# Kernel tuning notes

Hardware: AMD Instinct MI355X
Metric: run time of the kernel (lower is better)

## Reference

```python
import jax, jax.numpy as jnp
import numpy as np

NEG_SLOPE = 0.01  # torch F.leaky_relu default

def _leaky(x):
    return jnp.where(x >= 0, x, NEG_SLOPE * x)

def _gcn(x, W, b, src, dst, w, n):
    # GCNConv(add_self_loops=False, normalize=False):
    # h = x @ W; out[dst] += w * h[src]; out += b
    h = x @ W
    agg = jax.ops.segment_sum(w[:, None] * h[src], dst, num_segments=n)
    return agg + b

def setup_inputs() -> dict:
    key = jax.random.key(0)
    ks = jax.random.split(key, 10)
    N, E, IN, HID, OUT, B = 100000, 300000, 256, 256, 256, 128
    features = jax.random.normal(ks[0], (N, IN), dtype=jnp.float32)
    values = jax.random.uniform(ks[1], (E,), dtype=jnp.float32)
    s = 1.0 / np.sqrt(IN)
    W1 = jax.random.normal(ks[2], (IN, HID), dtype=jnp.float32) * s
    b1 = jnp.zeros((HID,), dtype=jnp.float32)
    W2 = jax.random.normal(ks[3], (HID + IN, OUT), dtype=jnp.float32) * (1.0 / np.sqrt(HID + IN))
    b2 = jnp.zeros((OUT,), dtype=jnp.float32)
    Wl = jax.random.normal(ks[4], (HID + OUT, IN), dtype=jnp.float32) * (1.0 / np.sqrt(HID + OUT))
    bl = jnp.zeros((IN,), dtype=jnp.float32)
    adjs = jax.random.randint(ks[5], (2, E), 0, N, dtype=jnp.int64)
    batch = jnp.sort(jax.random.randint(ks[6], (N,), 0, B, dtype=jnp.int64))
    root_idx = jax.random.randint(ks[7], (B,), 0, N, dtype=jnp.int64)
    return {"features": features, "values": values, "W1": W1, "b1": b1,
            "W2": W2, "b2": b2, "Wl": Wl, "bl": bl,
            "adjs": adjs, "batch": batch, "root_idx": root_idx}

def reference(features, values, W1, b1, W2, b2, Wl, bl, adjs, batch, root_idx):
    N = features.shape[0]
    src, dst = adjs[0], adjs[1]
    f1 = features  # [N, in]
    h = _gcn(f1, W1, b1, src, dst, values, N)  # conv1 -> [N, hid]
    f2 = h
    # root_extend: per-batch broadcast of root features == gather f1[root_idx[batch]]
    root1 = f1[root_idx[batch]]  # [N, in]
    x = _leaky(jnp.concatenate([h, root1], axis=1))
    # dropout is identity at inference
    x = _gcn(x, W2, b2, src, dst, values, N)  # conv2 -> [N, out]
    x = _leaky(x)
    root2 = f2[root_idx[batch]]  # [N, hid]
    x = jnp.concatenate([x, root2], axis=1)
    return _leaky(x @ Wl + bl)  # [N, in]
```

## Files before the change

### kernel.cpp

```cpp
#include <hip/hip_runtime.h>

typedef short short8 __attribute__((ext_vector_type(8)));
typedef float floatx4 __attribute__((ext_vector_type(4)));

#define LEAKY(v) ((v) >= 0.0f ? (v) : 0.01f * (v))

constexpr int D = 256;

__device__ __forceinline__ short f2bf(float x) {
  unsigned u = __float_as_uint(x);
  u += 0x7fffu + ((u >> 16) & 1u);
  return (short)(u >> 16);
}
__device__ __forceinline__ float bf2f(short s) {
  return __uint_as_float(((unsigned)(unsigned short)s) << 16);
}

#define AS1 __attribute__((address_space(1)))
#define AS3 __attribute__((address_space(3)))

__device__ __forceinline__ void gload_lds16(const void* g, void* lds) {
  __builtin_amdgcn_global_load_lds((const AS1 void*)g, (AS3 void*)lds, 16, 0, 0);
}

__global__ void transpose_w(const float* __restrict__ W1,
                            const float* __restrict__ W2,
                            const float* __restrict__ Wl,
                            short* __restrict__ Wt) {
  __shared__ float t[32][33];
  const float* src = (blockIdx.z == 0) ? W1 : (blockIdx.z == 1) ? W2 : Wl;
  short* dst = Wt + (size_t)blockIdx.z * D * D;
  int tx = threadIdx.x, ty = threadIdx.y;
  t[ty][tx] = src[(size_t)(blockIdx.y * 32 + ty) * D + blockIdx.x * 32 + tx];
  __syncthreads();
  dst[(size_t)(blockIdx.x * 32 + ty) * D + blockIdx.y * 32 + tx] =
      f2bf(t[tx][ty]);
}

template <bool A_F32, bool ADD_ROW, bool FINAL>
__global__ __launch_bounds__(512, 2) void gemm_pipe(
    const void* __restrict__ Avoid, const short* __restrict__ Wt,
    const float* __restrict__ R, const int* __restrict__ batch,
    const float* __restrict__ bias, void* __restrict__ Cvoid, int M,
    int nTiles) {
  constexpr int TB = A_F32 ? 32768 : 16384;
  __shared__ __align__(16) char As[2][TB];
  const int tid = threadIdx.x;
  const int l = tid & 63, w = tid >> 6, lm = l & 15, q = l >> 4;
  const int ncol0 = w * 32;

  short8 bf[2][8];
#pragma unroll
  for (int j = 0; j < 2; j++)
#pragma unroll
    for (int kk = 0; kk < 8; kk++)
      bf[j][kk] = *(const short8*)(Wt + (size_t)(ncol0 + j * 16 + lm) * D +
                                   kk * 32 + q * 8);
#pragma unroll
  for (int j = 0; j < 2; j++)
#pragma unroll
    for (int kk = 0; kk < 8; kk++)
      asm volatile("" : "+v"(bf[j][kk]));

  float4 b4[2];
  if (FINAL) {
#pragma unroll
    for (int j = 0; j < 2; j++)
      b4[j] = *(const float4*)(bias + ncol0 + j * 16 + q * 4);
  }

  const int stride = gridDim.x;
  int t = blockIdx.x;
  int p = 0;

  auto stage = [&](int tile, int buf) {
    if (A_F32) {
#pragma unroll
      for (int r = 0; r < 4; r++) {
        const int c = r * 8 + w;
        const int s = c >> 1, h = c & 1;
        const int kk = s >> 1, i = s & 1;
        int grow = tile * 32 + i * 16 + lm;
        grow = grow < M ? grow : M - 1;
        const char* src = (const char*)Avoid + (size_t)grow * 1024 +
                          kk * 128 + q * 32 + h * 16;
        gload_lds16(src, &As[buf][s * 2048 + h * 1024]);
      }
    } else {
#pragma unroll
      for (int r = 0; r < 2; r++) {
        const int s = r * 8 + w;
        const int kk = s >> 1, i = s & 1;
        int grow = tile * 32 + i * 16 + lm;
        grow = grow < M ? grow : M - 1;
        const char* src =
            (const char*)Avoid + (size_t)grow * 512 + kk * 64 + q * 16;
        gload_lds16(src, &As[buf][s * 1024]);
      }
    }
  };

  if (t < nTiles) stage(t, 0);

  for (; t < nTiles; t += stride) {
    __syncthreads();
    const int nxt = t + stride;
    if (nxt < nTiles) stage(nxt, p ^ 1);

    floatx4 acc[2][2];
#pragma unroll
    for (int i = 0; i < 2; i++)
#pragma unroll
      for (int j = 0; j < 2; j++) acc[i][j] = (floatx4){0.f, 0.f, 0.f, 0.f};

    const char* base = &As[p][0] + (size_t)l * 16;
#pragma unroll
    for (int kk = 0; kk < 8; kk++) {
      short8 a[2];
#pragma unroll
      for (int i = 0; i < 2; i++) {
        if (A_F32) {
          const int s = kk * 2 + i;
          float4 lo = *(const float4*)(base + s * 2048);
          float4 hi = *(const float4*)(base + s * 2048 + 1024);
          short8 sv;
          sv[0] = f2bf(lo.x); sv[1] = f2bf(lo.y); sv[2] = f2bf(lo.z); sv[3] = f2bf(lo.w);
          sv[4] = f2bf(hi.x); sv[5] = f2bf(hi.y); sv[6] = f2bf(hi.z); sv[7] = f2bf(hi.w);
          a[i] = sv;
        } else {
          a[i] = *(const short8*)(base + (kk * 2 + i) * 1024);
        }
      }
#pragma unroll
      for (int i = 0; i < 2; i++)
#pragma unroll
        for (int j = 0; j < 2; j++)
          acc[i][j] = __builtin_amdgcn_mfma_f32_16x16x32_bf16(
              bf[j][kk], a[i], acc[i][j], 0, 0, 0);
    }

    const int rowBase = t * 32;
#pragma unroll
    for (int i = 0; i < 2; i++) {
      const int row = rowBase + i * 16 + lm;
      if (row < M) {
        int rb = 0;
        if (ADD_ROW) rb = batch[row];
#pragma unroll
        for (int j = 0; j < 2; j++) {
          const int col0 = ncol0 + j * 16 + q * 4;
          float c0 = acc[i][j][0], c1 = acc[i][j][1], c2 = acc[i][j][2],
                c3 = acc[i][j][3];
          if (ADD_ROW) {
            float4 rv = *(const float4*)(R + (size_t)rb * D + col0);
            c0 += rv.x; c1 += rv.y; c2 += rv.z; c3 += rv.w;
          }
          if (!FINAL) {
            uint2 o;
            o.x = (unsigned)(unsigned short)f2bf(c0) |
                  ((unsigned)(unsigned short)f2bf(c1) << 16);
            o.y = (unsigned)(unsigned short)f2bf(c2) |
                  ((unsigned)(unsigned short)f2bf(c3) << 16);
            *(uint2*)((short*)Cvoid + (size_t)row * D + col0) = o;
          } else {
            c0 += b4[j].x; c1 += b4[j].y; c2 += b4[j].z; c3 += b4[j].w;
            c0 = LEAKY(c0); c1 = LEAKY(c1); c2 = LEAKY(c2); c3 = LEAKY(c3);
            float4 o = {c0, c1, c2, c3};
            *(float4*)((float*)Cvoid + (size_t)row * D + col0) = o;
          }
        }
      }
    }
    p ^= 1;
  }
}

__global__ void count_dst(const int* __restrict__ dst, int* __restrict__ offs,
                          int E) {
  int e = blockIdx.x * 256 + threadIdx.x;
  if (e < E) atomicAdd(&offs[dst[e]], 1);
}

__global__ void scan_blocks(int* __restrict__ offs, int* __restrict__ bsums,
                            int n) {
  __shared__ int tmp[256];
  int i = blockIdx.x * 256 + threadIdx.x;
  int v = (i < n) ? offs[i] : 0;
  tmp[threadIdx.x] = v;
  __syncthreads();
  for (int off = 1; off < 256; off <<= 1) {
    int t = (threadIdx.x >= off) ? tmp[threadIdx.x - off] : 0;
    __syncthreads();
    tmp[threadIdx.x] += t;
    __syncthreads();
  }
  if (i < n) offs[i] = tmp[threadIdx.x] - v;
  if (threadIdx.x == 255) bsums[blockIdx.x] = tmp[255];
}

__global__ void scan_sums(int* __restrict__ bs, int nb) {
  __shared__ int tmp[1024];
  int v = (threadIdx.x < nb) ? bs[threadIdx.x] : 0;
  tmp[threadIdx.x] = v;
  __syncthreads();
  for (int off = 1; off < 1024; off <<= 1) {
    int t = (threadIdx.x >= off) ? tmp[threadIdx.x - off] : 0;
    __syncthreads();
    tmp[threadIdx.x] += t;
    __syncthreads();
  }
  if (threadIdx.x < nb) bs[threadIdx.x] = tmp[threadIdx.x] - v;
}

__global__ void add_offsets(int* __restrict__ offs, const int* __restrict__ bs,
                            int n, int* __restrict__ cursor) {
  int i = blockIdx.x * 256 + threadIdx.x;
  if (i < n) {
    int o = offs[i] + bs[blockIdx.x];
    offs[i] = o;
    cursor[i] = o;
  }
}

__global__ void fill_buckets(const int* __restrict__ src,
                             const int* __restrict__ dst,
                             const float* __restrict__ vals,
                             int* __restrict__ cursor, int* __restrict__ esrc,
                             float* __restrict__ ew, int E) {
  int e = blockIdx.x * 256 + threadIdx.x;
  if (e < E) {
    int p = atomicAdd(&cursor[dst[e]], 1);
    esrc[p] = src[e];
    ew[p] = vals[e];
  }
}

__global__ __launch_bounds__(256) void aggregate_bf(
    const short* __restrict__ H, const int* __restrict__ offs,
    const int* __restrict__ esrc, const float* __restrict__ ew,
    const float* __restrict__ bias, short* __restrict__ out, int N, int E) {
  int node = blockIdx.x * 4 + (threadIdx.x >> 6);
  if (node >= N) return;
  const int lane = threadIdx.x & 63;
  const int half = lane >> 5, li = lane & 31;
  int beg = offs[node];
  int end = (node == N - 1) ? E : offs[node + 1];
  float a0 = 0.f, a1 = 0.f, a2 = 0.f, a3 = 0.f, a4 = 0.f, a5 = 0.f,
        a6 = 0.f, a7 = 0.f;
  for (int i = beg; i < end; i += 2) {
    const int idx = i + half;
    const bool v = idx < end;
    int s = esrc[v ? idx : i];
    float wv = v ? ew[idx] : 0.f;
    uint4 pk = *(const uint4*)(H + (size_t)s * D + li * 8);
    a0 += wv * bf2f((short)(pk.x & 0xffff));
    a1 += wv * bf2f((short)(pk.x >> 16));
    a2 += wv * bf2f((short)(pk.y & 0xffff));
    a3 += wv * bf2f((short)(pk.y >> 16));
    a4 += wv * bf2f((short)(pk.z & 0xffff));
    a5 += wv * bf2f((short)(pk.z >> 16));
    a6 += wv * bf2f((short)(pk.w & 0xffff));
    a7 += wv * bf2f((short)(pk.w >> 16));
  }
  a0 += __shfl_xor(a0, 32); a1 += __shfl_xor(a1, 32);
  a2 += __shfl_xor(a2, 32); a3 += __shfl_xor(a3, 32);
  a4 += __shfl_xor(a4, 32); a5 += __shfl_xor(a5, 32);
  a6 += __shfl_xor(a6, 32); a7 += __shfl_xor(a7, 32);
  if (half == 0) {
    float4 b0 = *(const float4*)(bias + li * 8);
    float4 b1 = *(const float4*)(bias + li * 8 + 4);
    a0 = LEAKY(a0 + b0.x); a1 = LEAKY(a1 + b0.y);
    a2 = LEAKY(a2 + b0.z); a3 = LEAKY(a3 + b0.w);
    a4 = LEAKY(a4 + b1.x); a5 = LEAKY(a5 + b1.y);
    a6 = LEAKY(a6 + b1.z); a7 = LEAKY(a7 + b1.w);
    uint4 o;
    o.x = (unsigned)(unsigned short)f2bf(a0) |
          ((unsigned)(unsigned short)f2bf(a1) << 16);
    o.y = (unsigned)(unsigned short)f2bf(a2) |
          ((unsigned)(unsigned short)f2bf(a3) << 16);
    o.z = (unsigned)(unsigned short)f2bf(a4) |
          ((unsigned)(unsigned short)f2bf(a5) << 16);
    o.w = (unsigned)(unsigned short)f2bf(a6) |
          ((unsigned)(unsigned short)f2bf(a7) << 16);
    *(uint4*)(out + (size_t)node * D + li * 8) = o;
  }
}

__global__ void root_both(const float* __restrict__ X,
                          const int* __restrict__ root_idx,
                          const float* __restrict__ W2, float* __restrict__ R1,
                          const short* __restrict__ H,
                          const int* __restrict__ offs,
                          const int* __restrict__ esrc,
                          const float* __restrict__ ew,
                          const float* __restrict__ b1,
                          const float* __restrict__ Wl, float* __restrict__ R2,
                          int N, int E, int B) {
  __shared__ float a[D];
  int j = threadIdx.x;
  if ((int)blockIdx.x < B) {
    int b = blockIdx.x;
    int r = root_idx[b];
    a[j] = LEAKY(X[(size_t)r * D + j]);
    __syncthreads();
    float acc = 0.f;
#pragma unroll 8
    for (int k = 0; k < D; k++) acc += a[k] * W2[(size_t)(D + k) * D + j];
    R1[b * D + j] = acc;
  } else {
    int b = blockIdx.x - B;
    int r = root_idx[b];
    int beg = offs[r], end = (r == N - 1) ? E : offs[r + 1];
    float acc = b1[j];
    for (int e = beg; e < end; e++)
      acc += ew[e] * bf2f(H[(size_t)esrc[e] * D + j]);
    a[j] = acc;
    __syncthreads();
    float s = 0.f;
#pragma unroll 8
    for (int k = 0; k < D; k++) s += a[k] * Wl[(size_t)(D + k) * D + j];
    R2[b * D + j] = s;
  }
}

extern "C" void kernel_launch(void* const* d_in, const int* in_sizes, int n_in,
                              void* d_out, int out_size, void* d_ws,
                              size_t ws_size, hipStream_t stream) {
  const float* features = (const float*)d_in[0];
  const float* values   = (const float*)d_in[1];
  const float* W1 = (const float*)d_in[2];
  const float* b1 = (const float*)d_in[3];
  const float* W2 = (const float*)d_in[4];
  const float* b2 = (const float*)d_in[5];
  const float* Wl = (const float*)d_in[6];
  const float* bl = (const float*)d_in[7];
  const int* adjs = (const int*)d_in[8];
  const int* batch = (const int*)d_in[9];
  const int* root_idx = (const int*)d_in[10];

  const int N = in_sizes[0] / D;
  const int E = in_sizes[1];
  const int B = in_sizes[10];
  const int* srcI = adjs;
  const int* dstI = adjs + E;

  short* bf0 = (short*)d_ws;
  short* bf1 = bf0 + (size_t)N * D;
  short* Wt = bf1 + (size_t)N * D;
  float* R1 = (float*)(Wt + (size_t)3 * D * D);
  float* R2 = R1 + (size_t)B * D;
  float* ew = R2 + (size_t)B * D;
  int* offs = (int*)(ew + E);
  int* cursor = offs + N;
  int* esrc = cursor + N;
  int* bsums = esrc + E;

  const int nb = (N + 255) / 256;

  hipMemsetAsync(offs, 0, (size_t)N * sizeof(int), stream);
  count_dst<<<(E + 255) / 256, 256, 0, stream>>>(dstI, offs, E);
  scan_blocks<<<nb, 256, 0, stream>>>(offs, bsums, N);
  scan_sums<<<1, 1024, 0, stream>>>(bsums, nb);
  add_offsets<<<nb, 256, 0, stream>>>(offs, bsums, N, cursor);
  fill_buckets<<<(E + 255) / 256, 256, 0, stream>>>(srcI, dstI, values, cursor,
                                                    esrc, ew, E);

  transpose_w<<<dim3(8, 8, 3), dim3(32, 32), 0, stream>>>(W1, W2, Wl, Wt);

  const int nTiles = (N + 31) / 32;
  const int ggrid = 512;
  const int aggGrid = (N + 3) / 4;

  gemm_pipe<true, false, false><<<ggrid, 512, 0, stream>>>(
      features, Wt, nullptr, nullptr, nullptr, bf0, N, nTiles);

  aggregate_bf<<<aggGrid, 256, 0, stream>>>(bf0, offs, esrc, ew, b1, bf1, N, E);

  root_both<<<2 * B, 256, 0, stream>>>(features, root_idx, W2, R1, bf0, offs,
                                       esrc, ew, b1, Wl, R2, N, E, B);

  gemm_pipe<false, true, false><<<ggrid, 512, 0, stream>>>(
      bf1, Wt + (size_t)D * D, R1, batch, nullptr, bf0, N, nTiles);

  aggregate_bf<<<aggGrid, 256, 0, stream>>>(bf0, offs, esrc, ew, b2, bf1, N, E);

  gemm_pipe<false, true, true><<<ggrid, 512, 0, stream>>>(
      bf1, Wt + (size_t)2 * D * D, R2, batch, bl, (float*)d_out, N, nTiles);
}
```

Baseline: 419.1 us.

## Replace persistent register-resident-W GEMM with 128x128 LDS-tiled GEMM

The persistent GEMM kernel kept a 32-column slice of the weight matrix in registers, used double-buffered 32-row A tiles, and ran 512 threads per block. It is replaced by a non-persistent kernel where each 256-thread block computes a 128x128 output tile. Both A and B are staged through LDS in K-chunks of 64, and each wave computes a 4x4 grid of MFMA tiles. The goal is more arithmetic per LDS load and better data reuse. In exchange it drops the cross-tile prefetch overlap, adds a synchronize on every K step, and re-reads the weights from global memory and L2 in every block.

```diff
diff --git a/kernel.cpp b/kernel.cpp
--- a/kernel.cpp
+++ b/kernel.cpp
@@ -38,140 +38,122 @@
 }
 
 template <bool A_F32, bool ADD_ROW, bool FINAL>
-__global__ __launch_bounds__(512, 2) void gemm_pipe(
+__global__ __launch_bounds__(256, 3) void gemm_tile(
     const void* __restrict__ Avoid, const short* __restrict__ Wt,
     const float* __restrict__ R, const int* __restrict__ batch,
-    const float* __restrict__ bias, void* __restrict__ Cvoid, int M,
-    int nTiles) {
-  constexpr int TB = A_F32 ? 32768 : 16384;
-  __shared__ __align__(16) char As[2][TB];
+    const float* __restrict__ bias, void* __restrict__ Cvoid, int M) {
+  constexpr int ABYTES = A_F32 ? 32768 : 16384;
+  __shared__ __align__(16) char As[ABYTES];
+  __shared__ __align__(16) char Bs[16384];
   const int tid = threadIdx.x;
   const int l = tid & 63, w = tid >> 6, lm = l & 15, q = l >> 4;
-  const int ncol0 = w * 32;
-
-  short8 bf[2][8];
-#pragma unroll
-  for (int j = 0; j < 2; j++)
-#pragma unroll
-    for (int kk = 0; kk < 8; kk++)
-      bf[j][kk] = *(const short8*)(Wt + (size_t)(ncol0 + j * 16 + lm) * D +
-                                   kk * 32 + q * 8);
-#pragma unroll
-  for (int j = 0; j < 2; j++)
-#pragma unroll
-    for (int kk = 0; kk < 8; kk++)
-      asm volatile("" : "+v"(bf[j][kk]));
-
-  float4 b4[2];
-  if (FINAL) {
-#pragma unroll
-    for (int j = 0; j < 2; j++)
-      b4[j] = *(const float4*)(bias + ncol0 + j * 16 + q * 4);
-  }
-
-  const int stride = gridDim.x;
-  int t = blockIdx.x;
-  int p = 0;
-
-  auto stage = [&](int tile, int buf) {
+  const int wr = w >> 1, wc = w & 1;
+  const int rowBase = (blockIdx.x >> 1) * 128;
+  const int colTile = (blockIdx.x & 1) * 128;
+
+  floatx4 acc[4][4];
+#pragma unroll
+  for (int i = 0; i < 4; i++)
+#pragma unroll
+    for (int j = 0; j < 4; j++) acc[i][j] = (floatx4){0.f, 0.f, 0.f, 0.f};
+
+  for (int k0 = 0; k0 < 256; k0 += 64) {
     if (A_F32) {
 #pragma unroll
-      for (int r = 0; r < 4; r++) {
-        const int c = r * 8 + w;
+      for (int r = 0; r < 8; r++) {
+        const int c = r * 4 + w;
         const int s = c >> 1, h = c & 1;
-        const int kk = s >> 1, i = s & 1;
-        int grow = tile * 32 + i * 16 + lm;
+        const int kk = s >> 3, ar = (s >> 2) & 1, i = s & 3;
+        int grow = rowBase + ar * 64 + i * 16 + lm;
         grow = grow < M ? grow : M - 1;
-        const char* src = (const char*)Avoid + (size_t)grow * 1024 +
+        const char* src = (const char*)Avoid + (size_t)grow * 1024 + k0 * 4 +
                           kk * 128 + q * 32 + h * 16;
-        gload_lds16(src, &As[buf][s * 2048 + h * 1024]);
+        gload_lds16(src, As + s * 2048 + h * 1024);
       }
     } else {
 #pragma unroll
-      for (int r = 0; r < 2; r++) {
-        const int s = r * 8 + w;
-        const int kk = s >> 1, i = s & 1;
-        int grow = tile * 32 + i * 16 + lm;
+      for (int r = 0; r < 4; r++) {
+        const int c = r * 4 + w;
+        const int kk = c >> 3, ar = (c >> 2) & 1, i = c & 3;
+        int grow = rowBase + ar * 64 + i * 16 + lm;
         grow = grow < M ? grow : M - 1;
-        const char* src =
-            (const char*)Avoid + (size_t)grow * 512 + kk * 64 + q * 16;
-        gload_lds16(src, &As[buf][s * 1024]);
+        const char* src = (const char*)Avoid + (size_t)grow * 512 + k0 * 2 +
+                          kk * 64 + q * 16;
+        gload_lds16(src, As + c * 1024);
       }
     }
-  };
-
-  if (t < nTiles) stage(t, 0);
-
-  for (; t < nTiles; t += stride) {
-    __syncthreads();
-    const int nxt = t + stride;
-    if (nxt < nTiles) stage(nxt, p ^ 1);
-
-    floatx4 acc[2][2];
-#pragma unroll
-    for (int i = 0; i < 2; i++)
-#pragma unroll
-      for (int j = 0; j < 2; j++) acc[i][j] = (floatx4){0.f, 0.f, 0.f, 0.f};
-
-    const char* base = &As[p][0] + (size_t)l * 16;
-#pragma unroll
-    for (int kk = 0; kk < 8; kk++) {
-      short8 a[2];
-#pragma unroll
-      for (int i = 0; i < 2; i++) {
+#pragma unroll
+    for (int r = 0; r < 4; r++) {
+      const int c = r * 4 + w;
+      const int kk = c >> 3, bc = (c >> 2) & 1, j = c & 3;
+      const int gn = colTile + bc * 64 + j * 16 + lm;
+      const char* src =
+          (const char*)Wt + (size_t)gn * 512 + k0 * 2 + kk * 64 + q * 16;
+      gload_lds16(src, Bs + c * 1024);
+    }
+    __syncthreads();
+
+#pragma unroll
+    for (int kk = 0; kk < 2; kk++) {
+      short8 a[4], b[4];
+#pragma unroll
+      for (int i = 0; i < 4; i++) {
         if (A_F32) {
-          const int s = kk * 2 + i;
-          float4 lo = *(const float4*)(base + s * 2048);
-          float4 hi = *(const float4*)(base + s * 2048 + 1024);
+          const int s = kk * 8 + wr * 4 + i;
+          float4 lo = *(const float4*)(As + s * 2048 + l * 16);
+          float4 hi = *(const float4*)(As + s * 2048 + 1024 + l * 16);
           short8 sv;
           sv[0] = f2bf(lo.x); sv[1] = f2bf(lo.y); sv[2] = f2bf(lo.z); sv[3] = f2bf(lo.w);
           sv[4] = f2bf(hi.x); sv[5] = f2bf(hi.y); sv[6] = f2bf(hi.z); sv[7] = f2bf(hi.w);
           a[i] = sv;
         } else {
-          a[i] = *(const short8*)(base + (kk * 2 + i) * 1024);
+          a[i] = *(const short8*)(As + (kk * 8 + wr * 4 + i) * 1024 + l * 16);
         }
       }
 #pragma unroll
-      for (int i = 0; i < 2; i++)
-#pragma unroll
-        for (int j = 0; j < 2; j++)
-          acc[i][j] = __builtin_amdgcn_mfma_f32_16x16x32_bf16(
-              bf[j][kk], a[i], acc[i][j], 0, 0, 0);
+      for (int j = 0; j < 4; j++)
+        b[j] = *(const short8*)(Bs + (kk * 8 + wc * 4 + j) * 1024 + l * 16);
+#pragma unroll
+      for (int i = 0; i < 4; i++)
+#pragma unroll
+        for (int j = 0; j < 4; j++)
+          acc[i][j] = __builtin_amdgcn_mfma_f32_16x16x32_bf16(b[j], a[i],
+                                                              acc[i][j], 0, 0, 0);
     }
-
-    const int rowBase = t * 32;
-#pragma unroll
-    for (int i = 0; i < 2; i++) {
-      const int row = rowBase + i * 16 + lm;
-      if (row < M) {
-        int rb = 0;
-        if (ADD_ROW) rb = batch[row];
-#pragma unroll
-        for (int j = 0; j < 2; j++) {
-          const int col0 = ncol0 + j * 16 + q * 4;
-          float c0 = acc[i][j][0], c1 = acc[i][j][1], c2 = acc[i][j][2],
-                c3 = acc[i][j][3];
-          if (ADD_ROW) {
-            float4 rv = *(const float4*)(R + (size_t)rb * D + col0);
-            c0 += rv.x; c1 += rv.y; c2 += rv.z; c3 += rv.w;
-          }
-          if (!FINAL) {
-            uint2 o;
-            o.x = (unsigned)(unsigned short)f2bf(c0) |
-                  ((unsigned)(unsigned short)f2bf(c1) << 16);
-            o.y = (unsigned)(unsigned short)f2bf(c2) |
-                  ((unsigned)(unsigned short)f2bf(c3) << 16);
-            *(uint2*)((short*)Cvoid + (size_t)row * D + col0) = o;
-          } else {
-            c0 += b4[j].x; c1 += b4[j].y; c2 += b4[j].z; c3 += b4[j].w;
-            c0 = LEAKY(c0); c1 = LEAKY(c1); c2 = LEAKY(c2); c3 = LEAKY(c3);
-            float4 o = {c0, c1, c2, c3};
-            *(float4*)((float*)Cvoid + (size_t)row * D + col0) = o;
-          }
+    __syncthreads();
+  }
+
+#pragma unroll
+  for (int i = 0; i < 4; i++) {
+    const int row = rowBase + wr * 64 + i * 16 + lm;
+    if (row < M) {
+      int rb = 0;
+      if (ADD_ROW) rb = batch[row];
+#pragma unroll
+      for (int j = 0; j < 4; j++) {
+        const int col0 = colTile + wc * 64 + j * 16 + q * 4;
+        float c0 = acc[i][j][0], c1 = acc[i][j][1], c2 = acc[i][j][2],
+              c3 = acc[i][j][3];
+        if (ADD_ROW) {
+          float4 rv = *(const float4*)(R + (size_t)rb * D + col0);
+          c0 += rv.x; c1 += rv.y; c2 += rv.z; c3 += rv.w;
+        }
+        if (!FINAL) {
+          uint2 o;
+          o.x = (unsigned)(unsigned short)f2bf(c0) |
+                ((unsigned)(unsigned short)f2bf(c1) << 16);
+          o.y = (unsigned)(unsigned short)f2bf(c2) |
+                ((unsigned)(unsigned short)f2bf(c3) << 16);
+          *(uint2*)((short*)Cvoid + (size_t)row * D + col0) = o;
+        } else {
+          float4 bv = *(const float4*)(bias + col0);
+          c0 += bv.x; c1 += bv.y; c2 += bv.z; c3 += bv.w;
+          c0 = LEAKY(c0); c1 = LEAKY(c1); c2 = LEAKY(c2); c3 = LEAKY(c3);
+          float4 o = {c0, c1, c2, c3};
+          *(float4*)((float*)Cvoid + (size_t)row * D + col0) = o;
         }
       }
     }
-    p ^= 1;
   }
 }
 
@@ -367,23 +349,22 @@
 
   transpose_w<<<dim3(8, 8, 3), dim3(32, 32), 0, stream>>>(W1, W2, Wl, Wt);
 
-  const int nTiles = (N + 31) / 32;
-  const int ggrid = 512;
+  const int ggrid = ((N + 127) / 128) * 2;
   const int aggGrid = (N + 3) / 4;
 
-  gemm_pipe<true, false, false><<<ggrid, 512, 0, stream>>>(
-      features, Wt, nullptr, nullptr, nullptr, bf0, N, nTiles);
+  gemm_tile<true, false, false><<<ggrid, 256, 0, stream>>>(
+      features, Wt, nullptr, nullptr, nullptr, bf0, N);
 
   aggregate_bf<<<aggGrid, 256, 0, stream>>>(bf0, offs, esrc, ew, b1, bf1, N, E);
 
   root_both<<<2 * B, 256, 0, stream>>>(features, root_idx, W2, R1, bf0, offs,
                                        esrc, ew, b1, Wl, R2, N, E, B);
 
-  gemm_pipe<false, true, false><<<ggrid, 512, 0, stream>>>(
-      bf1, Wt + (size_t)D * D, R1, batch, nullptr, bf0, N, nTiles);
+  gemm_tile<false, true, false><<<ggrid, 256, 0, stream>>>(
+      bf1, Wt + (size_t)D * D, R1, batch, nullptr, bf0, N);
 
   aggregate_bf<<<aggGrid, 256, 0, stream>>>(bf0, offs, esrc, ew, b2, bf1, N, E);
 
-  gemm_pipe<false, true, true><<<ggrid, 512, 0, stream>>>(
-      bf1, Wt + (size_t)2 * D * D, R2, batch, bl, (float*)d_out, N, nTiles);
-}
+  gemm_tile<false, true, true><<<ggrid, 256, 0, stream>>>(
+      bf1, Wt + (size_t)2 * D * D, R2, batch, bl, (float*)d_out, N);
+}
```

Result: slower. 450.7 us (+7.5%).
